# Kernel optimization log

Measured on AMD Instinct MI355X. Metric: run time of the kernel, lower is better.

Reference implementation:

```python
import jax, jax.numpy as jnp
import numpy as np

DEPTH = 4
HEADS = 8
DIM = 512
HID = 1024  # int(512 * 2.0)
P = 16
IMG = 224
GRID = IMG // P          # 14
NPATCH = GRID * GRID     # 196
NTOK = NPATCH + 1        # 197 (cls token)
BATCH = 64
EPS = 1e-5               # torch LayerNorm default


def layernorm(x, w, b):
    mu = jnp.mean(x, axis=-1, keepdims=True)
    var = jnp.mean(jnp.square(x - mu), axis=-1, keepdims=True)
    return (x - mu) * jax.lax.rsqrt(var + EPS) * w + b


def setup_inputs() -> dict:
    key = jax.random.key(0)
    ks = jax.random.split(key, 12)
    s = 0.02
    inp = {
        "x": jax.random.normal(ks[0], (BATCH, 3, IMG, IMG), jnp.float32),
        # patch-embed conv as matmul: kernel flattened in torch order (c, kh, kw)
        "conv_w": jax.random.normal(ks[1], (3 * P * P, DIM), jnp.float32) * s,
        "conv_b": jnp.zeros((DIM,), jnp.float32),
        "cls_token": jax.random.normal(ks[2], (1, 1, DIM), jnp.float32) * s,
        "pos_embed": jax.random.normal(ks[3], (1, NTOK, DIM), jnp.float32) * s,
        # per-block params stacked along depth
        "ln1_w": jnp.ones((DEPTH, DIM), jnp.float32),
        "ln1_b": jnp.zeros((DEPTH, DIM), jnp.float32),
        "qkv_w": jax.random.normal(ks[4], (DEPTH, DIM, 3 * DIM), jnp.float32) * s,
        "qkv_b": jnp.zeros((DEPTH, 3 * DIM), jnp.float32),
        "proj_w": jax.random.normal(ks[5], (DEPTH, DIM, DIM), jnp.float32) * s,
        "proj_b": jnp.zeros((DEPTH, DIM), jnp.float32),
        "ln2_w": jnp.ones((DEPTH, DIM), jnp.float32),
        "ln2_b": jnp.zeros((DEPTH, DIM), jnp.float32),
        "fc1_w": jax.random.normal(ks[6], (DEPTH, DIM, HID), jnp.float32) * s,
        "fc1_b": jnp.zeros((DEPTH, HID), jnp.float32),
        "fc2_w": jax.random.normal(ks[7], (DEPTH, HID, DIM), jnp.float32) * s,
        "fc2_b": jnp.zeros((DEPTH, DIM), jnp.float32),
        "norm_w": jnp.ones((DIM,), jnp.float32),
        "norm_b": jnp.zeros((DIM,), jnp.float32),
    }
    return inp


def reference(x, conv_w, conv_b, cls_token, pos_embed,
              ln1_w, ln1_b, qkv_w, qkv_b, proj_w, proj_b,
              ln2_w, ln2_b, fc1_w, fc1_b, fc2_w, fc2_b,
              norm_w, norm_b):
    B = x.shape[0]
    hd = DIM // HEADS
    scale = hd ** -0.5
    # PatchEmbed: conv with kernel=stride=patch == patch extraction + matmul
    patches = x.reshape(B, 3, GRID, P, GRID, P)
    patches = patches.transpose(0, 2, 4, 1, 3, 5).reshape(B, NPATCH, 3 * P * P)
    tok = patches @ conv_w + conv_b                      # [B, 196, DIM]
    cls = jnp.broadcast_to(cls_token, (B, 1, DIM))
    h = jnp.concatenate([cls, tok], axis=1) + pos_embed  # [B, 197, DIM]
    for i in range(DEPTH):
        # Attention block (eval mode: dropouts are identity)
        y = layernorm(h, ln1_w[i], ln1_b[i])
        qkv = (y @ qkv_w[i] + qkv_b[i]).reshape(B, NTOK, 3, HEADS, hd)
        qkv = qkv.transpose(2, 0, 3, 1, 4)               # [3, B, H, N, hd]
        q, k, v = qkv[0], qkv[1], qkv[2]
        attn = jax.nn.softmax(jnp.einsum('bhnd,bhmd->bhnm', q, k) * scale, axis=-1)
        o = jnp.einsum('bhnm,bhmd->bhnd', attn, v)
        o = o.transpose(0, 2, 1, 3).reshape(B, NTOK, DIM)
        h = h + (o @ proj_w[i] + proj_b[i])
        # MLP block (exact GELU as in torch nn.GELU)
        y = layernorm(h, ln2_w[i], ln2_b[i])
        y = jax.nn.gelu(y @ fc1_w[i] + fc1_b[i], approximate=False)
        h = h + (y @ fc2_w[i] + fc2_b[i])
    return layernorm(h, norm_w, norm_b)
```

## Files before the change

kernel.cpp:

```cpp
#include <hip/hip_runtime.h>
#include <hip/hip_bf16.h>

#define HEADS 8
#define DIM 512
#define HID 1024
#define NTOK 197
#define NPATCH 196
#define BATCH 64
#define MTOK (BATCH*NTOK)
#define MPATCH (BATCH*NPATCH)
#define KPATCH 768

typedef __attribute__((ext_vector_type(8))) short vbf8;
typedef __attribute__((ext_vector_type(4))) float vf4;

__device__ inline float bf2f(short u) {
  union { unsigned int i; float f; } v; v.i = ((unsigned int)(unsigned short)u) << 16; return v.f;
}
__device__ inline short f2bf(float f) {
  union { float f; unsigned int i; } u; u.f = f;
  unsigned int r = u.i + 0x7fffu + ((u.i >> 16) & 1u);
  return (short)(r >> 16);
}

__device__ inline void gl_lds16(const void* g, void* l) {
  __builtin_amdgcn_global_load_lds(
      (const __attribute__((address_space(1))) void*)g,
      (__attribute__((address_space(3))) void*)l, 16, 0, 0);
}

__global__ void k_cvt_t(const float* __restrict__ in, short* __restrict__ out, int K, int N) {
  int slice = blockIdx.z;
  in  += (size_t)slice * K * N;
  out += (size_t)slice * K * N;
  __shared__ short tile[64][72];
  int t = threadIdx.x;
  int k0 = blockIdx.y * 64, n0 = blockIdx.x * 64;
  int r = t >> 2, c4 = (t & 3) << 4;
  #pragma unroll
  for (int j = 0; j < 16; j += 4) {
    float4 v = *(const float4*)(in + (size_t)(k0 + r) * N + n0 + c4 + j);
    tile[r][c4 + j + 0] = f2bf(v.x);
    tile[r][c4 + j + 1] = f2bf(v.y);
    tile[r][c4 + j + 2] = f2bf(v.z);
    tile[r][c4 + j + 3] = f2bf(v.w);
  }
  __syncthreads();
  int n = t >> 2, kc = (t & 3) << 4;
  vbf8 a, b;
  #pragma unroll
  for (int j = 0; j < 8; ++j) a[j] = tile[kc + j][n];
  #pragma unroll
  for (int j = 0; j < 8; ++j) b[j] = tile[kc + 8 + j][n];
  *(vbf8*)(out + (size_t)(n0 + n) * K + k0 + kc) = a;
  *(vbf8*)(out + (size_t)(n0 + n) * K + k0 + kc + 8) = b;
}

__global__ void k_im2col(const float* __restrict__ x, short* __restrict__ patches) {
  int tid = blockIdx.x * 256 + threadIdx.x;
  if (tid >= MPATCH * 48) return;
  int b = tid / (NPATCH * 48);
  int r = tid % (NPATCH * 48);
  int p = r / 48;
  int ck = r % 48;
  int c = ck >> 4, kh = ck & 15;
  int gy = p / 14, gx = p % 14;
  const float* src = x + ((size_t)((b * 3 + c) * 224) + gy * 16 + kh) * 224 + gx * 16;
  short* dst = patches + (size_t)(b * NPATCH + p) * KPATCH + c * 256 + kh * 16;
  float4 v0 = *(const float4*)(src);
  float4 v1 = *(const float4*)(src + 4);
  float4 v2 = *(const float4*)(src + 8);
  float4 v3 = *(const float4*)(src + 12);
  vbf8 o0, o1;
  o0[0]=f2bf(v0.x); o0[1]=f2bf(v0.y); o0[2]=f2bf(v0.z); o0[3]=f2bf(v0.w);
  o0[4]=f2bf(v1.x); o0[5]=f2bf(v1.y); o0[6]=f2bf(v1.z); o0[7]=f2bf(v1.w);
  o1[0]=f2bf(v2.x); o1[1]=f2bf(v2.y); o1[2]=f2bf(v2.z); o1[3]=f2bf(v2.w);
  o1[4]=f2bf(v3.x); o1[5]=f2bf(v3.y); o1[6]=f2bf(v3.z); o1[7]=f2bf(v3.w);
  *(vbf8*)dst = o0;
  *(vbf8*)(dst + 8) = o1;
}

__global__ void k_cls(const float* __restrict__ cls, const float* __restrict__ pos,
                      float* __restrict__ h) {
  int b = blockIdx.x, t = threadIdx.x;
  float* hr = h + (size_t)b * NTOK * DIM;
  hr[t]       = cls[t]       + pos[t];
  hr[t + 256] = cls[t + 256] + pos[t + 256];
}

template<int OUTBF>
__global__ void k_ln(const float* __restrict__ x, const float* __restrict__ w,
                     const float* __restrict__ b, void* __restrict__ out) {
  int row = blockIdx.x;
  int t = threadIdx.x;
  const float* xr = x + (size_t)row * DIM;
  float2 v = *(const float2*)(xr + t * 2);
  float s = v.x + v.y;
  float ss = v.x * v.x + v.y * v.y;
  #pragma unroll
  for (int o = 32; o > 0; o >>= 1) { s += __shfl_down(s, o); ss += __shfl_down(ss, o); }
  __shared__ float sm[8];
  int wid = t >> 6, lane = t & 63;
  if (lane == 0) { sm[wid] = s; sm[4 + wid] = ss; }
  __syncthreads();
  if (t == 0) {
    float a = sm[0] + sm[1] + sm[2] + sm[3];
    float q = sm[4] + sm[5] + sm[6] + sm[7];
    float mu = a * (1.0f / DIM);
    float var = q * (1.0f / DIM) - mu * mu;
    sm[0] = mu; sm[1] = rsqrtf(var + 1e-5f);
  }
  __syncthreads();
  float mu = sm[0], rs = sm[1];
  float2 wv = *(const float2*)(w + t * 2);
  float2 bv = *(const float2*)(b + t * 2);
  float y0 = (v.x - mu) * rs * wv.x + bv.x;
  float y1 = (v.y - mu) * rs * wv.y + bv.y;
  if (OUTBF) {
    unsigned int pk = (unsigned short)f2bf(y0) | ((unsigned int)(unsigned short)f2bf(y1) << 16);
    ((unsigned int*)out)[(size_t)row * (DIM / 2) + t] = pk;
  } else {
    float2 o2; o2.x = y0; o2.y = y1;
    *((float2*)out + (size_t)row * (DIM / 2) + t) = o2;
  }
}

template<int MODE>
__global__ __launch_bounds__(256) void k_gemm(
    const short* __restrict__ A, const short* __restrict__ Bt,
    const float* __restrict__ bias, void* __restrict__ out,
    const float* __restrict__ extra, int M, int N, int K)
{
  __shared__ short As[128 * 64];
  __shared__ short Bs[128 * 64];
  int bn = blockIdx.x, bm = blockIdx.y;
  int t = threadIdx.x, wid = t >> 6, lane = t & 63;
  int wm = wid >> 1, wn = wid & 1;
  int lr = lane & 15, lk = lane >> 4;
  int srow = lane >> 3;
  int scol = (lane & 7) * 8;
  vf4 zero4; zero4[0] = 0.f; zero4[1] = 0.f; zero4[2] = 0.f; zero4[3] = 0.f;
  vf4 acc[4][4];
  #pragma unroll
  for (int i = 0; i < 4; ++i)
    #pragma unroll
    for (int j = 0; j < 4; ++j) acc[i][j] = zero4;

  for (int k0 = 0; k0 < K; k0 += 64) {
    if (k0) __syncthreads();
    #pragma unroll
    for (int i = 0; i < 4; ++i) {
      int rc = wid * 4 + i;
      gl_lds16(A  + (size_t)(bm * 128 + rc * 8 + srow) * K + k0 + scol, As + rc * 512);
      gl_lds16(Bt + (size_t)(bn * 128 + rc * 8 + srow) * K + k0 + scol, Bs + rc * 512);
    }
    __syncthreads();
    #pragma unroll
    for (int s = 0; s < 2; ++s) {
      vbf8 af[4], bfr[4];
      #pragma unroll
      for (int i = 0; i < 4; ++i)
        af[i] = *(const vbf8*)&As[(wm * 64 + i * 16 + lr) * 64 + s * 32 + lk * 8];
      #pragma unroll
      for (int j = 0; j < 4; ++j)
        bfr[j] = *(const vbf8*)&Bs[(wn * 64 + j * 16 + lr) * 64 + s * 32 + lk * 8];
      #pragma unroll
      for (int i = 0; i < 4; ++i)
        #pragma unroll
        for (int j = 0; j < 4; ++j)
          acc[i][j] = __builtin_amdgcn_mfma_f32_16x16x32_bf16(af[i], bfr[j], acc[i][j], 0, 0, 0);
    }
  }

  int rbase = bm * 128 + wm * 64;
  int cbase = bn * 128 + wn * 64;
  #pragma unroll
  for (int i = 0; i < 4; ++i) {
    #pragma unroll
    for (int j = 0; j < 4; ++j) {
      int col = cbase + j * 16 + lr;
      float bs = bias[col];
      #pragma unroll
      for (int z = 0; z < 4; ++z) {
        int row = rbase + i * 16 + lk * 4 + z;
        if (row < M) {
          float v = acc[i][j][z] + bs;
          if (MODE == 0) {
            ((short*)out)[(size_t)row * N + col] = f2bf(v);
          } else if (MODE == 1) {
            float g = 0.5f * v * (1.f + erff(v * 0.70710678118f));
            ((short*)out)[(size_t)row * N + col] = f2bf(g);
          } else if (MODE == 2) {
            float* hp = (float*)out + (size_t)row * N + col;
            *hp = *hp + v;
          } else {
            int b_ = row / NPATCH, p = row - b_ * NPATCH;
            ((float*)out)[((size_t)b_ * NTOK + 1 + p) * DIM + col] =
                v + extra[(size_t)(1 + p) * DIM + col];
          }
        }
      }
    }
  }
}

#define VSTR 232
__global__ __launch_bounds__(256) void k_attn(const short* __restrict__ qkv,
                                              short* __restrict__ o) {
  int h = blockIdx.x, b = blockIdx.y;
  __shared__ short Vt[64 * VSTR];
  __shared__ short Pt[4][16 * VSTR];
  int t = threadIdx.x, wid = t >> 6, lane = t & 63;
  int lq = lane & 15, g4 = lane >> 4;
  const size_t base = (size_t)(b * NTOK) * 1536 + h * 64;

  vbf8 vz;
  #pragma unroll
  for (int j = 0; j < 8; ++j) vz[j] = 0;
  for (int idx = t; idx < 224 * 8; idx += 256) {
    int r = idx >> 3, c8 = idx & 7;
    vbf8 v = vz;
    if (r < NTOK) v = *(const vbf8*)(qkv + base + (size_t)r * 1536 + 1024 + c8 * 8);
    int cs = r ^ ((c8 & 3) << 3);
    #pragma unroll
    for (int j = 0; j < 8; ++j) Vt[(c8 * 8 + j) * VSTR + cs] = v[j];
  }
  __syncthreads();

  short* Pw = &Pt[wid][0];
  for (int qt = wid; qt < 13; qt += 4) {
    const short* qp = qkv + base + (size_t)(qt * 16 + lq) * 1536 + g4 * 8;
    vbf8 qf0 = *(const vbf8*)qp;
    vbf8 qf1 = *(const vbf8*)(qp + 32);
    float sc[13][4];
    #pragma unroll
    for (int kt = 0; kt < 13; ++kt) {
      const short* kp = qkv + base + (size_t)(kt * 16 + lq) * 1536 + 512 + g4 * 8;
      vbf8 kf0 = *(const vbf8*)kp;
      vbf8 kf1 = *(const vbf8*)(kp + 32);
      vf4 s; s[0] = 0.f; s[1] = 0.f; s[2] = 0.f; s[3] = 0.f;
      s = __builtin_amdgcn_mfma_f32_16x16x32_bf16(kf0, qf0, s, 0, 0, 0);
      s = __builtin_amdgcn_mfma_f32_16x16x32_bf16(kf1, qf1, s, 0, 0, 0);
      #pragma unroll
      for (int z = 0; z < 4; ++z) {
        int krow = kt * 16 + g4 * 4 + z;
        sc[kt][z] = (krow < NTOK) ? s[z] * 0.125f : -1e30f;
      }
    }
    float mx = -1e30f;
    #pragma unroll
    for (int kt = 0; kt < 13; ++kt)
      #pragma unroll
      for (int z = 0; z < 4; ++z) mx = fmaxf(mx, sc[kt][z]);
    mx = fmaxf(mx, __shfl_xor(mx, 16));
    mx = fmaxf(mx, __shfl_xor(mx, 32));
    float sum = 0.f;
    #pragma unroll
    for (int kt = 0; kt < 13; ++kt)
      #pragma unroll
      for (int z = 0; z < 4; ++z) {
        float e = __expf(sc[kt][z] - mx);
        sc[kt][z] = e;
        sum += e;
      }
    sum += __shfl_xor(sum, 16);
    sum += __shfl_xor(sum, 32);
    float inv = 1.f / sum;
    #pragma unroll
    for (int kt = 0; kt < 13; ++kt) {
      *(short4*)&Pw[lq * VSTR + kt * 16 + g4 * 4] =
          make_short4(f2bf(sc[kt][0]), f2bf(sc[kt][1]), f2bf(sc[kt][2]), f2bf(sc[kt][3]));
    }
    *(short4*)&Pw[lq * VSTR + 208 + g4 * 4] = make_short4(0, 0, 0, 0);
    vf4 oacc[4];
    #pragma unroll
    for (int dt = 0; dt < 4; ++dt) { oacc[dt][0]=0.f; oacc[dt][1]=0.f; oacc[dt][2]=0.f; oacc[dt][3]=0.f; }
    #pragma unroll
    for (int u = 0; u < 7; ++u) {
      vbf8 pb = *(const vbf8*)&Pw[lq * VSTR + u * 32 + g4 * 8];
      #pragma unroll
      for (int dt = 0; dt < 4; ++dt) {
        int swz = ((dt * 2 + (lq >> 3)) & 3) << 3;
        vbf8 va = *(const vbf8*)&Vt[(dt * 16 + lq) * VSTR + ((u * 32 + g4 * 8) ^ swz)];
        oacc[dt] = __builtin_amdgcn_mfma_f32_16x16x32_bf16(va, pb, oacc[dt], 0, 0, 0);
      }
    }
    int qrow = qt * 16 + lq;
    if (qrow < NTOK) {
      short* op = o + ((size_t)(b * NTOK) + qrow) * DIM + h * 64 + g4 * 4;
      #pragma unroll
      for (int dt = 0; dt < 4; ++dt)
        *(short4*)(op + dt * 16) = make_short4(f2bf(oacc[dt][0] * inv), f2bf(oacc[dt][1] * inv),
                                               f2bf(oacc[dt][2] * inv), f2bf(oacc[dt][3] * inv));
    }
  }
}

extern "C" void kernel_launch(void* const* d_in, const int* in_sizes, int n_in,
                              void* d_out, int out_size, void* d_ws, size_t ws_size,
                              hipStream_t stream) {
  (void)in_sizes; (void)n_in; (void)out_size; (void)ws_size;
  const float* x      = (const float*)d_in[0];
  const float* conv_w = (const float*)d_in[1];
  const float* conv_b = (const float*)d_in[2];
  const float* cls    = (const float*)d_in[3];
  const float* pos    = (const float*)d_in[4];
  const float* ln1_w  = (const float*)d_in[5];
  const float* ln1_b  = (const float*)d_in[6];
  const float* qkv_w  = (const float*)d_in[7];
  const float* qkv_b  = (const float*)d_in[8];
  const float* proj_w = (const float*)d_in[9];
  const float* proj_b = (const float*)d_in[10];
  const float* ln2_w  = (const float*)d_in[11];
  const float* ln2_b  = (const float*)d_in[12];
  const float* fc1_w  = (const float*)d_in[13];
  const float* fc1_b  = (const float*)d_in[14];
  const float* fc2_w  = (const float*)d_in[15];
  const float* fc2_b  = (const float*)d_in[16];
  const float* norm_w = (const float*)d_in[17];
  const float* norm_b = (const float*)d_in[18];

  short* conv_wT = (short*)d_ws;
  short* qkv_wT  = conv_wT + (size_t)512 * 768;
  short* proj_wT = qkv_wT  + (size_t)4 * 1536 * 512;
  short* fc1_wT  = proj_wT + (size_t)4 * 512 * 512;
  short* fc2_wT  = fc1_wT  + (size_t)4 * 512 * 1024;
  short* y_bf    = fc2_wT  + (size_t)4 * 1024 * 512;
  short* o_bf    = y_bf    + (size_t)MTOK * 512;
  short* big     = o_bf    + (size_t)MTOK * 512;
  float* h       = (float*)(big + (size_t)MTOK * 1536);

  k_cvt_t<<<dim3(8, 12, 1), 256, 0, stream>>>(conv_w, conv_wT, 768, 512);
  k_cvt_t<<<dim3(24, 8, 4), 256, 0, stream>>>(qkv_w, qkv_wT, 512, 1536);
  k_cvt_t<<<dim3(8, 8, 4), 256, 0, stream>>>(proj_w, proj_wT, 512, 512);
  k_cvt_t<<<dim3(16, 8, 4), 256, 0, stream>>>(fc1_w, fc1_wT, 512, 1024);
  k_cvt_t<<<dim3(8, 16, 4), 256, 0, stream>>>(fc2_w, fc2_wT, 1024, 512);

  k_im2col<<<2352, 256, 0, stream>>>(x, big);
  k_cls<<<64, 256, 0, stream>>>(cls, pos, h);
  k_gemm<3><<<dim3(4, 98), 256, 0, stream>>>(big, conv_wT, conv_b, h, pos,
                                             MPATCH, 512, 768);
  for (int i = 0; i < 4; ++i) {
    k_ln<1><<<MTOK, 256, 0, stream>>>(h, ln1_w + i * 512, ln1_b + i * 512, y_bf);
    k_gemm<0><<<dim3(12, 99), 256, 0, stream>>>(y_bf, qkv_wT + (size_t)i * 512 * 1536,
                                                qkv_b + i * 1536, big, nullptr,
                                                MTOK, 1536, 512);
    k_attn<<<dim3(8, 64), 256, 0, stream>>>(big, o_bf);
    k_gemm<2><<<dim3(4, 99), 256, 0, stream>>>(o_bf, proj_wT + (size_t)i * 512 * 512,
                                               proj_b + i * 512, h, nullptr,
                                               MTOK, 512, 512);
    k_ln<1><<<MTOK, 256, 0, stream>>>(h, ln2_w + i * 512, ln2_b + i * 512, y_bf);
    k_gemm<1><<<dim3(8, 99), 256, 0, stream>>>(y_bf, fc1_wT + (size_t)i * 512 * 1024,
                                               fc1_b + i * 1024, big, nullptr,
                                               MTOK, 1024, 512);
    k_gemm<2><<<dim3(4, 99), 256, 0, stream>>>(big, fc2_wT + (size_t)i * 1024 * 512,
                                               fc2_b + i * 512, h, nullptr,
                                               MTOK, 512, 1024);
  }
  k_ln<0><<<MTOK, 256, 0, stream>>>(h, norm_w, norm_b, d_out);
}
```

Measured before the change: 952.6 us.

## Double-buffer GEMM LDS tiles and use narrower N tiles for N=512 GEMMs

The GEMM kernel now keeps two LDS buffers for the A and B tiles and issues the next K-tile's global-to-LDS loads before computing on the current one, so there is one barrier per iteration instead of two. This is meant to overlap memory loads with MFMA work. The N tile width is now a template parameter: the N=512 GEMMs (patch embed, proj, fc2) use 64-wide tiles, doubling their grid to give more blocks across the CUs. The cost is double the LDS per block, which may limit occupancy, and more redundant loads of A for the narrower tiles.

```diff
diff --git a/kernel.cpp b/kernel.cpp
--- a/kernel.cpp
+++ b/kernel.cpp
@@ -125,59 +125,77 @@
   }
 }
 
-template<int MODE>
+template<int MODE, int BNF>
 __global__ __launch_bounds__(256) void k_gemm(
     const short* __restrict__ A, const short* __restrict__ Bt,
     const float* __restrict__ bias, void* __restrict__ out,
     const float* __restrict__ extra, int M, int N, int K)
 {
-  __shared__ short As[128 * 64];
-  __shared__ short Bs[128 * 64];
+  constexpr int BN = BNF * 32;
+  __shared__ short As[2][128 * 64];
+  __shared__ short Bs[2][BN * 64];
   int bn = blockIdx.x, bm = blockIdx.y;
   int t = threadIdx.x, wid = t >> 6, lane = t & 63;
   int wm = wid >> 1, wn = wid & 1;
   int lr = lane & 15, lk = lane >> 4;
   int srow = lane >> 3;
   int scol = (lane & 7) * 8;
-  vf4 zero4; zero4[0] = 0.f; zero4[1] = 0.f; zero4[2] = 0.f; zero4[3] = 0.f;
-  vf4 acc[4][4];
-  #pragma unroll
-  for (int i = 0; i < 4; ++i)
-    #pragma unroll
-    for (int j = 0; j < 4; ++j) acc[i][j] = zero4;
-
-  for (int k0 = 0; k0 < K; k0 += 64) {
-    if (k0) __syncthreads();
+
+  const short* Abase = A  + (size_t)(bm * 128 + srow) * K + scol;
+  const short* Bbase = Bt + (size_t)(bn * BN  + srow) * K + scol;
+
+  auto stage = [&](int buf, int k0) {
     #pragma unroll
     for (int i = 0; i < 4; ++i) {
       int rc = wid * 4 + i;
-      gl_lds16(A  + (size_t)(bm * 128 + rc * 8 + srow) * K + k0 + scol, As + rc * 512);
-      gl_lds16(Bt + (size_t)(bn * 128 + rc * 8 + srow) * K + k0 + scol, Bs + rc * 512);
-    }
-    __syncthreads();
+      gl_lds16(Abase + (size_t)(rc * 8) * K + k0, &As[buf][rc * 512]);
+    }
+    #pragma unroll
+    for (int i = 0; i < BNF; ++i) {
+      int rc = wid * BNF + i;
+      gl_lds16(Bbase + (size_t)(rc * 8) * K + k0, &Bs[buf][rc * 512]);
+    }
+  };
+
+  vf4 acc[4][BNF];
+  #pragma unroll
+  for (int i = 0; i < 4; ++i)
+    #pragma unroll
+    for (int j = 0; j < BNF; ++j) {
+      acc[i][j][0] = 0.f; acc[i][j][1] = 0.f; acc[i][j][2] = 0.f; acc[i][j][3] = 0.f;
+    }
+
+  int nt = K >> 6;
+  stage(0, 0);
+  __syncthreads();
+  int cur = 0;
+  for (int tt = 0; tt < nt; ++tt) {
+    if (tt + 1 < nt) stage(cur ^ 1, (tt + 1) << 6);
     #pragma unroll
     for (int s = 0; s < 2; ++s) {
-      vbf8 af[4], bfr[4];
+      vbf8 af[4], bfr[BNF];
       #pragma unroll
       for (int i = 0; i < 4; ++i)
-        af[i] = *(const vbf8*)&As[(wm * 64 + i * 16 + lr) * 64 + s * 32 + lk * 8];
-      #pragma unroll
-      for (int j = 0; j < 4; ++j)
-        bfr[j] = *(const vbf8*)&Bs[(wn * 64 + j * 16 + lr) * 64 + s * 32 + lk * 8];
+        af[i] = *(const vbf8*)&As[cur][(wm * 64 + i * 16 + lr) * 64 + s * 32 + lk * 8];
+      #pragma unroll
+      for (int j = 0; j < BNF; ++j)
+        bfr[j] = *(const vbf8*)&Bs[cur][(wn * (BN / 2) + j * 16 + lr) * 64 + s * 32 + lk * 8];
       #pragma unroll
       for (int i = 0; i < 4; ++i)
         #pragma unroll
-        for (int j = 0; j < 4; ++j)
+        for (int j = 0; j < BNF; ++j)
           acc[i][j] = __builtin_amdgcn_mfma_f32_16x16x32_bf16(af[i], bfr[j], acc[i][j], 0, 0, 0);
     }
+    __syncthreads();
+    cur ^= 1;
   }
 
   int rbase = bm * 128 + wm * 64;
-  int cbase = bn * 128 + wn * 64;
+  int cbase = bn * BN + wn * (BN / 2);
   #pragma unroll
   for (int i = 0; i < 4; ++i) {
     #pragma unroll
-    for (int j = 0; j < 4; ++j) {
+    for (int j = 0; j < BNF; ++j) {
       int col = cbase + j * 16 + lr;
       float bs = bias[col];
       #pragma unroll
@@ -338,24 +356,24 @@
 
   k_im2col<<<2352, 256, 0, stream>>>(x, big);
   k_cls<<<64, 256, 0, stream>>>(cls, pos, h);
-  k_gemm<3><<<dim3(4, 98), 256, 0, stream>>>(big, conv_wT, conv_b, h, pos,
-                                             MPATCH, 512, 768);
+  k_gemm<3, 2><<<dim3(8, 98), 256, 0, stream>>>(big, conv_wT, conv_b, h, pos,
+                                                MPATCH, 512, 768);
   for (int i = 0; i < 4; ++i) {
     k_ln<1><<<MTOK, 256, 0, stream>>>(h, ln1_w + i * 512, ln1_b + i * 512, y_bf);
-    k_gemm<0><<<dim3(12, 99), 256, 0, stream>>>(y_bf, qkv_wT + (size_t)i * 512 * 1536,
-                                                qkv_b + i * 1536, big, nullptr,
-                                                MTOK, 1536, 512);
+    k_gemm<0, 4><<<dim3(12, 99), 256, 0, stream>>>(y_bf, qkv_wT + (size_t)i * 512 * 1536,
+                                                   qkv_b + i * 1536, big, nullptr,
+                                                   MTOK, 1536, 512);
     k_attn<<<dim3(8, 64), 256, 0, stream>>>(big, o_bf);
-    k_gemm<2><<<dim3(4, 99), 256, 0, stream>>>(o_bf, proj_wT + (size_t)i * 512 * 512,
-                                               proj_b + i * 512, h, nullptr,
-                                               MTOK, 512, 512);
+    k_gemm<2, 2><<<dim3(8, 99), 256, 0, stream>>>(o_bf, proj_wT + (size_t)i * 512 * 512,
+                                                  proj_b + i * 512, h, nullptr,
+                                                  MTOK, 512, 512);
     k_ln<1><<<MTOK, 256, 0, stream>>>(h, ln2_w + i * 512, ln2_b + i * 512, y_bf);
-    k_gemm<1><<<dim3(8, 99), 256, 0, stream>>>(y_bf, fc1_wT + (size_t)i * 512 * 1024,
-                                               fc1_b + i * 1024, big, nullptr,
-                                               MTOK, 1024, 512);
-    k_gemm<2><<<dim3(4, 99), 256, 0, stream>>>(big, fc2_wT + (size_t)i * 1024 * 512,
-                                               fc2_b + i * 512, h, nullptr,
-                                               MTOK, 512, 1024);
+    k_gemm<1, 4><<<dim3(8, 99), 256, 0, stream>>>(y_bf, fc1_wT + (size_t)i * 512 * 1024,
+                                                  fc1_b + i * 1024, big, nullptr,
+                                                  MTOK, 1024, 512);
+    k_gemm<2, 2><<<dim3(8, 99), 256, 0, stream>>>(big, fc2_wT + (size_t)i * 1024 * 512,
+                                                  fc2_b + i * 512, h, nullptr,
+                                                  MTOK, 512, 1024);
   }
   k_ln<0><<<MTOK, 256, 0, stream>>>(h, norm_w, norm_b, d_out);
 }
```

Result: slower. 1.105 ms (+16.0%).
